# Kernel tuning notes

Hardware: AMD Instinct MI355X
Metric: run time of the kernel (lower is better)

## Reference

```python
import jax, jax.numpy as jnp
import numpy as np

BOS, PAD, EOS, UNK = 0, 1, 2, 3  # fairseq dictionary special-token ids
CHAR_VOCAB = 5000
DIM = 512
LATENT = 10000


def setup_inputs() -> dict:
    key = jax.random.key(0)
    k1, k2, k3 = jax.random.split(key, 3)
    # char-ngram ids per token: [B, T, max_char_len]
    x = jax.random.randint(k1, (8, 1024, 20), 0, CHAR_VOCAB, dtype=jnp.int64 if jax.config.jax_enable_x64 else jnp.int32)
    # char ngram embedding table (also serves as preset_emb for special tokens)
    char_table = jax.random.normal(k2, (CHAR_VOCAB, DIM), dtype=jnp.float32) * 0.05
    # fixed latent codebook, init std = latent**-0.5 as in the module
    latent_mat = jax.random.normal(k3, (LATENT, DIM), dtype=jnp.float32) * (LATENT ** -0.5)
    return {"x": x, "char_table": char_table, "latent_mat": latent_mat}


def reference(x, char_table, latent_mat):
    # --- CharacterNgramEmbedder: gather + sum-pool over char ngrams (pad masked) ---
    emb = char_table[x]                                   # [B, T, C, D]
    valid = (x != PAD)[..., None].astype(emb.dtype)       # pad ngrams contribute 0
    ngram_weight = jnp.sum(emb * valid, axis=2)           # [B, T, D]
    lang_emb = jnp.tanh(ngram_weight)

    # --- latent codebook attention: QK^T -> softmax -> V over fixed codebook ---
    latent_scores = jnp.einsum('btd,ld->btl', lang_emb, latent_mat)   # [B, T, L]
    latent_dist = jax.nn.softmax(latent_scores, axis=-1)
    latent_emb = jnp.einsum('btl,ld->btd', latent_dist, latent_mat)   # [B, T, D]
    sde_emb = lang_emb + latent_emb

    # --- preset_emb overwrite for special tokens (masked scatter) ---
    first = x[:, :, 0]                                    # [B, T]
    for tok in (PAD, BOS, EOS, UNK):
        sde_emb = jnp.where((first == tok)[..., None], char_table[tok], sde_emb)
    return sde_emb
```

## Files before the change

### kernel.cpp

```cpp
#include <hip/hip_runtime.h>

#define BT    8192
#define DIM   512
#define NLAT  10000
#define LPAD2 10240
#define NG    20
#define CV    5000

typedef short bf16x8 __attribute__((ext_vector_type(8)));
typedef float f32x4  __attribute__((ext_vector_type(4)));
typedef unsigned short u16;
typedef u16 u16x8 __attribute__((ext_vector_type(8)));
typedef u16 u16x4 __attribute__((ext_vector_type(4)));

static __device__ __forceinline__ u16 f2bf(float f) {
    union { float f; unsigned u; } v; v.f = f;
    unsigned r = v.u + 0x7FFF + ((v.u >> 16) & 1);
    return (u16)(r >> 16);
}
static __device__ __forceinline__ float bf2f(u16 b) {
    union { unsigned u; float f; } v; v.u = ((unsigned)b) << 16; return v.f;
}

static __device__ __forceinline__ void gload16(const void* g, void* l) {
    __builtin_amdgcn_global_load_lds(
        (const __attribute__((address_space(1))) unsigned int*)g,
        (__attribute__((address_space(3))) unsigned int*)l,
        16, 0, 0);
}

__global__ __launch_bounds__(256) void ct2bf_kernel(
        const float* __restrict__ ct, u16* __restrict__ ctb) {
    const long base = ((long)blockIdx.x * 256 + threadIdx.x) * 8;
    float4 a = *(const float4*)(ct + base);
    float4 b = *(const float4*)(ct + base + 4);
    u16x8 v = { f2bf(a.x), f2bf(a.y), f2bf(a.z), f2bf(a.w),
                f2bf(b.x), f2bf(b.y), f2bf(b.z), f2bf(b.w) };
    *(u16x8*)(ctb + base) = v;
}

__global__ __launch_bounds__(256) void lang_kernel(
        const int* __restrict__ x, const u16* __restrict__ ctb,
        float* __restrict__ lang, u16* __restrict__ qb) {
    const int wv  = threadIdx.x >> 6;
    const int tl  = threadIdx.x & 63;
    const int tok0 = blockIdx.x * 8 + wv * 2;
    const int* xr0 = x + tok0 * NG;
    const int* xr1 = xr0 + NG;
    float s0[8], s1[8];
    #pragma unroll
    for (int i = 0; i < 8; ++i) { s0[i] = 0.f; s1[i] = 0.f; }
    #pragma unroll
    for (int j = 0; j < NG; ++j) {
        int c0 = xr0[j], c1 = xr1[j];
        if (c0 != 1) {
            u16x8 v = *(const u16x8*)(ctb + (long)c0 * DIM + tl * 8);
            #pragma unroll
            for (int i = 0; i < 8; ++i) s0[i] += bf2f(v[i]);
        }
        if (c1 != 1) {
            u16x8 v = *(const u16x8*)(ctb + (long)c1 * DIM + tl * 8);
            #pragma unroll
            for (int i = 0; i < 8; ++i) s1[i] += bf2f(v[i]);
        }
    }
    #pragma unroll
    for (int p = 0; p < 2; ++p) {
        float* s = p ? s1 : s0;
        const long tok = tok0 + p;
        float4 lo, hi;
        lo.x = tanhf(s[0]); lo.y = tanhf(s[1]); lo.z = tanhf(s[2]); lo.w = tanhf(s[3]);
        hi.x = tanhf(s[4]); hi.y = tanhf(s[5]); hi.z = tanhf(s[6]); hi.w = tanhf(s[7]);
        *(float4*)(lang + tok * DIM + tl * 8)     = lo;
        *(float4*)(lang + tok * DIM + tl * 8 + 4) = hi;
        u16x8 o = { f2bf(lo.x), f2bf(lo.y), f2bf(lo.z), f2bf(lo.w),
                    f2bf(hi.x), f2bf(hi.y), f2bf(hi.z), f2bf(hi.w) };
        *(u16x8*)(qb + tok * DIM + tl * 8) = o;
    }
}

__global__ __launch_bounds__(256) void conv_kernel(
        const float* __restrict__ lm, u16* __restrict__ kvg, u16* __restrict__ latT) {
    __shared__ u16 tile[64][514];
    const int lb = blockIdx.x * 64;
    const int t  = threadIdx.x;

    #pragma unroll 4
    for (int i = 0; i < 16; ++i) {
        int ch  = t + i * 256;
        int r   = ch >> 6;
        int c8  = ch & 63;
        int row = lb + r;
        u16x8 v = {0,0,0,0,0,0,0,0};
        if (row < NLAT) {
            const float* src = lm + (long)row * DIM + c8 * 8;
            float4 a = *(const float4*)src;
            float4 b = *(const float4*)(src + 4);
            v[0]=f2bf(a.x); v[1]=f2bf(a.y); v[2]=f2bf(a.z); v[3]=f2bf(a.w);
            v[4]=f2bf(b.x); v[5]=f2bf(b.y); v[6]=f2bf(b.z); v[7]=f2bf(b.w);
        }
        *(u16x8*)(kvg + (long)row * DIM + c8 * 8) = v;
        #pragma unroll
        for (int j = 0; j < 8; ++j) tile[r][c8 * 8 + j] = v[j];
    }
    __syncthreads();
    #pragma unroll 4
    for (int i = 0; i < 16; ++i) {
        int ch = t + i * 256;
        int d  = ch >> 3;
        int c8 = ch & 7;
        u16x8 v;
        #pragma unroll
        for (int j = 0; j < 8; ++j) v[j] = tile[c8 * 8 + j][d];
        *(u16x8*)(latT + (long)d * LPAD2 + lb + c8 * 8) = v;
    }
}

#define G1_COMPUTE(buf) {                                                      \
    bf16x8 af_[4], bf_[4];                                                     \
    _Pragma("unroll")                                                          \
    for (int mf_ = 0; mf_ < 4; ++mf_) {                                        \
        const int rA_ = wm * 64 + mf_ * 16 + lr;                               \
        const int ck_ = g ^ ((rA_ >> 1) & 3);                                  \
        af_[mf_] = *(const bf16x8*)&lds[buf][rA_ * 32 + ck_ * 8];              \
    }                                                                          \
    _Pragma("unroll")                                                          \
    for (int nf_ = 0; nf_ < 4; ++nf_) {                                        \
        const int rB_ = wn * 64 + nf_ * 16 + lr;                               \
        const int ck_ = g ^ ((rB_ >> 1) & 3);                                  \
        bf_[nf_] = *(const bf16x8*)&lds[buf][8192 + rB_ * 32 + ck_ * 8];       \
    }                                                                          \
    __builtin_amdgcn_s_setprio(1);                                             \
    _Pragma("unroll")                                                          \
    for (int mf_ = 0; mf_ < 4; ++mf_)                                          \
        _Pragma("unroll")                                                      \
        for (int nf_ = 0; nf_ < 4; ++nf_)                                      \
            acc[mf_][nf_] = __builtin_amdgcn_mfma_f32_16x16x32_bf16(           \
                af_[mf_], bf_[nf_], acc[mf_][nf_], 0, 0, 0);                   \
    __builtin_amdgcn_s_setprio(0);                                             \
}

#define G1_STAGE(buf, kt) {                                                    \
    const int k0_ = (kt) * 32;                                                 \
    {                                                                          \
        int ch_ = t;                                                           \
        int row_ = ch_ >> 2, c2_ = ch_ & 3;                                    \
        int sc_ = (c2_ ^ ((row_ >> 1) & 3)) * 8;                               \
        gload16(Q + (m0 + row_) * (long)DIM + k0_ + sc_, &lds[buf][ch_ * 8]);  \
        ch_ = t + 512; row_ = ch_ >> 2; c2_ = ch_ & 3;                         \
        sc_ = (c2_ ^ ((row_ >> 1) & 3)) * 8;                                   \
        gload16(Q + (m0 + row_) * (long)DIM + k0_ + sc_, &lds[buf][ch_ * 8]);  \
        row_ = t >> 2; c2_ = t & 3;                                            \
        sc_ = (c2_ ^ ((row_ >> 1) & 3)) * 8;                                   \
        gload16(Bgp + (long)row_ * DIM + k0_ + sc_, &lds[buf][8192 + t * 8]);  \
    }                                                                          \
}

#define G1_STEP(kt, vmn) {                                                     \
    asm volatile("s_waitcnt vmcnt(" #vmn ")" ::: "memory");                    \
    __builtin_amdgcn_s_barrier();                                              \
    G1_COMPUTE((kt) % 3);                                                      \
    __builtin_amdgcn_s_barrier();                                              \
}

__global__ __launch_bounds__(512, 4) void gemm1_kernel(
        const u16* __restrict__ Q, const u16* __restrict__ L,
        u16* __restrict__ P, float* __restrict__ rowsum,
        int n0_global, int npanels, int pstride) {
    __shared__ u16 lds[3][12288];

    const int nwg = 32 * npanels;
    const int cpx = nwg >> 3;
    const int bid = blockIdx.x;
    const int wg  = (bid & 7) * cpx + (bid >> 3);
    int mb, nb;
    if (npanels == 80) {
        const int st = wg / 80, lt = wg % 80;
        const int lmb = lt & 7, lnb = lt >> 3;
        const int smb = st & 3, snb = st >> 2;
        mb = smb * 8 + lmb;
        nb = snb * 10 + lnb;
    } else {
        mb = wg & 31;
        nb = wg >> 5;
    }
    const long m0    = (long)mb * 256;
    const int  ncol0 = n0_global + nb * 128;

    const u16* Bgp = L + (long)ncol0 * DIM;

    const int t = threadIdx.x, lane = t & 63, w = t >> 6;
    const int wm = w >> 1, wn = w & 1;
    const int g = lane >> 4, lr = lane & 15;

    f32x4 acc[4][4];
    #pragma unroll
    for (int m = 0; m < 4; ++m)
        #pragma unroll
        for (int n = 0; n < 4; ++n) acc[m][n] = f32x4{0.f,0.f,0.f,0.f};

    G1_STAGE(0, 0);
    G1_STAGE(1, 1);
    G1_STAGE(2, 2);

    #pragma unroll 1
    for (int kt = 0; kt < 13; ++kt) {
        asm volatile("s_waitcnt vmcnt(6)" ::: "memory");
        __builtin_amdgcn_s_barrier();
        G1_COMPUTE(kt % 3);
        __builtin_amdgcn_s_barrier();
        G1_STAGE(kt % 3, kt + 3);
    }
    G1_STEP(13, 6);
    G1_STEP(14, 3);
    asm volatile("s_waitcnt vmcnt(0)" ::: "memory");
    __builtin_amdgcn_s_barrier();
    G1_COMPUTE(15 % 3);
    __syncthreads();

    u16* lds16 = &lds[0][0];
    #pragma unroll
    for (int mf = 0; mf < 4; ++mf)
        #pragma unroll
        for (int nf = 0; nf < 4; ++nf) {
            const int col = ncol0 + wn * 64 + nf * 16 + lr;
            const bool ok = (col < NLAT);
            const int lcol = wn * 64 + nf * 16 + lr;
            #pragma unroll
            for (int r = 0; r < 4; ++r) {
                float p = ok ? __expf(acc[mf][nf][r]) : 0.f;
                acc[mf][nf][r] = p;
                const int row = wm * 64 + mf * 16 + g * 4 + r;
                lds16[row * 128 + (lcol ^ ((row & 15) << 3))] = f2bf(p);
            }
        }

    #pragma unroll
    for (int mf = 0; mf < 4; ++mf) {
        float sv[4] = {0.f, 0.f, 0.f, 0.f};
        #pragma unroll
        for (int nf = 0; nf < 4; ++nf)
            #pragma unroll
            for (int r = 0; r < 4; ++r) sv[r] += acc[mf][nf][r];
        #pragma unroll
        for (int r = 0; r < 4; ++r) {
            float s = sv[r];
            s += __shfl_xor(s, 1); s += __shfl_xor(s, 2);
            s += __shfl_xor(s, 4); s += __shfl_xor(s, 8);
            if (lr == 0)
                atomicAdd(&rowsum[m0 + wm * 64 + mf * 16 + g * 4 + r], s);
        }
    }

    __syncthreads();
    const int pbase = ncol0 - n0_global;
    #pragma unroll
    for (int it = 0; it < 8; ++it) {
        const int flat = t + it * 512;
        const int row = flat >> 4, ck = flat & 15;
        u16x8 v = *(const u16x8*)&lds16[row * 128 + ((ck ^ (row & 15)) * 8)];
        *(u16x8*)(P + (m0 + row) * (long)pstride + pbase + ck * 8) = v;
    }
}

#define G2_STAGE(buf, kt) {                                                    \
    const int kloc_ = (step_off + (kt)) * 32;                                  \
    {                                                                          \
        int ch_ = t;                                                           \
        int row_ = ch_ >> 2, c2_ = ch_ & 3;                                    \
        int sc_ = (c2_ ^ ((row_ >> 1) & 3)) * 8;                               \
        gload16(P + (m0 + row_) * (long)pstride + kloc_ + sc_, &lds[buf][ch_ * 8]); \
        ch_ = t + 512; row_ = ch_ >> 2; c2_ = ch_ & 3;                         \
        sc_ = (c2_ ^ ((row_ >> 1) & 3)) * 8;                                   \
        gload16(P + (m0 + row_) * (long)pstride + kloc_ + sc_, &lds[buf][ch_ * 8]); \
        row_ = t >> 2; c2_ = t & 3;                                            \
        sc_ = (c2_ ^ ((row_ >> 1) & 3)) * 8;                                   \
        gload16(LT + (long)(nbase + row_) * LPAD2 + n0_global + kloc_ + sc_,   \
                &lds[buf][8192 + t * 8]);                                      \
    }                                                                          \
}

__global__ __launch_bounds__(512, 4) void gemm2_kernel(
        const u16* __restrict__ P, const u16* __restrict__ LT,
        float* __restrict__ out, float* __restrict__ parts,
        int pstride, int kcols, int n0_global, int splitk, int accum) {
    __shared__ u16 lds[3][12288];

    const int per = 4 * splitk;
    const int nwg = 32 * per;
    const int cpx = nwg >> 3;
    const int bid = blockIdx.x;
    const int wg  = (bid & 7) * cpx + (bid >> 3);
    const int mb  = wg / per;
    const int inr = wg % per;
    const int nb  = inr / splitk;
    const int s   = inr % splitk;

    const long m0    = (long)mb * 256;
    const int  nbase = nb * 128;

    const int nsteps = kcols / 32;
    const int q = nsteps / splitk, rr = nsteps % splitk;
    const int NT       = q + (s < rr ? 1 : 0);
    const int step_off = s * q + (s < rr ? s : rr);

    const int t = threadIdx.x, lane = t & 63, w = t >> 6;
    const int wm = w >> 1, wn = w & 1;
    const int g = lane >> 4, lr = lane & 15;

    float* buf = (s == 0) ? out : (parts + (long)(s - 1) * BT * DIM);

    f32x4 acc[4][4];
    #pragma unroll
    for (int m = 0; m < 4; ++m)
        #pragma unroll
        for (int n = 0; n < 4; ++n) acc[m][n] = f32x4{0.f,0.f,0.f,0.f};

    G2_STAGE(0, 0);
    G2_STAGE(1, 1);
    G2_STAGE(2, 2);

    #pragma unroll 1
    for (int kt = 0; kt < NT - 3; ++kt) {
        asm volatile("s_waitcnt vmcnt(6)" ::: "memory");
        __builtin_amdgcn_s_barrier();
        G1_COMPUTE(kt % 3);
        __builtin_amdgcn_s_barrier();
        G2_STAGE(kt % 3, kt + 3);
    }
    {
        asm volatile("s_waitcnt vmcnt(6)" ::: "memory");
        __builtin_amdgcn_s_barrier();
        G1_COMPUTE((NT - 3) % 3);
        __builtin_amdgcn_s_barrier();
    }
    {
        asm volatile("s_waitcnt vmcnt(3)" ::: "memory");
        __builtin_amdgcn_s_barrier();
        G1_COMPUTE((NT - 2) % 3);
        __builtin_amdgcn_s_barrier();
    }
    asm volatile("s_waitcnt vmcnt(0)" ::: "memory");
    __builtin_amdgcn_s_barrier();
    G1_COMPUTE((NT - 1) % 3);

    #pragma unroll
    for (int mf = 0; mf < 4; ++mf)
        #pragma unroll
        for (int nf = 0; nf < 4; ++nf) {
            const int col = nbase + wn * 64 + nf * 16 + lr;
            #pragma unroll
            for (int r = 0; r < 4; ++r) {
                const long row = m0 + wm * 64 + mf * 16 + g * 4 + r;
                float v = acc[mf][nf][r];
                if (accum) v += buf[row * DIM + col];
                buf[row * DIM + col] = v;
            }
        }
}

__global__ __launch_bounds__(256) void final_kernel(
        float* __restrict__ out, const float* __restrict__ parts,
        const float* __restrict__ lang, const float* __restrict__ rowsum,
        const int* __restrict__ x, const float* __restrict__ ct, int nparts) {
    const int tok   = blockIdx.x * 2 + (threadIdx.x >> 7);
    const int c4    = (threadIdx.x & 127) * 4;
    const long idx  = (long)tok * DIM + c4;
    const float inv = 1.f / rowsum[tok];
    const int first = x[tok * NG];

    float4 v = *(const float4*)(out + idx);
    for (int p = 1; p < nparts; ++p) {
        float4 pv = *(const float4*)(parts + (long)(p - 1) * BT * DIM + idx);
        v.x += pv.x; v.y += pv.y; v.z += pv.z; v.w += pv.w;
    }
    float4 lg = *(const float4*)(lang + idx);
    v.x = v.x * inv + lg.x; v.y = v.y * inv + lg.y;
    v.z = v.z * inv + lg.z; v.w = v.w * inv + lg.w;
    if (first < 4) v = *(const float4*)(ct + first * DIM + c4);
    *(float4*)(out + idx) = v;
}

extern "C" void kernel_launch(void* const* d_in, const int* in_sizes, int n_in,
                              void* d_out, int out_size, void* d_ws, size_t ws_size,
                              hipStream_t stream) {
    const int*   x  = (const int*)d_in[0];
    const float* ct = (const float*)d_in[1];
    const float* lm = (const float*)d_in[2];
    float* out = (float*)d_out;

    char* ws = (char*)d_ws;
    size_t off = 0;
    u16*   qb   = (u16*)(ws + off);   off += (size_t)BT * DIM * 2;
    float* lang = (float*)(ws + off); off += (size_t)BT * DIM * 4;
    u16*   kvg  = (u16*)(ws + off);   off += (size_t)LPAD2 * DIM * 2;
    u16*   latT = (u16*)(ws + off);   off += (size_t)DIM * LPAD2 * 2;
    u16*   ctb  = (u16*)(ws + off);   off += (size_t)CV * DIM * 2;
    float* rowsum = (float*)(ws + off); off += (size_t)BT * 4;
    u16*   P    = (u16*)(ws + off);
    const size_t fixed = off;

    const int panels_total = LPAD2 / 128;
    const size_t pfull = (size_t)BT * LPAD2 * 2;
    const size_t partb = (size_t)BT * DIM * 4;

    int splitk = 1, ppc = panels_total;
    float* parts = out;
    if (ws_size >= fixed + pfull + 3 * partb) {
        splitk = 4;
        parts = (float*)(ws + fixed + pfull);
    } else if (ws_size >= fixed + pfull + partb) {
        splitk = 2;
        parts = (float*)(ws + fixed + pfull);
    } else if (ws_size >= fixed + pfull) {
        splitk = 1;
    } else {
        size_t avail = (ws_size > fixed) ? (ws_size - fixed) : 0;
        size_t p = avail / ((size_t)BT * 128 * 2);
        ppc = (int)(p < 1 ? 1 : (p > (size_t)panels_total ? (size_t)panels_total : p));
        if (ppc & 1) ppc = (ppc > 1) ? ppc - 1 : 1;
    }
    const int pstride = ppc * 128;

    hipMemsetAsync(rowsum, 0, (size_t)BT * 4, stream);
    ct2bf_kernel<<<CV * DIM / (256 * 8), 256, 0, stream>>>(ct, ctb);
    lang_kernel<<<BT / 8, 256, 0, stream>>>(x, ctb, lang, qb);
    conv_kernel<<<LPAD2 / 64, 256, 0, stream>>>(lm, kvg, latT);

    int chunk = 0;
    for (int cs = 0; cs < panels_total; cs += ppc, ++chunk) {
        const int np = (panels_total - cs < ppc) ? (panels_total - cs) : ppc;
        gemm1_kernel<<<32 * np, 512, 0, stream>>>(qb, kvg, P, rowsum,
                                                  cs * 128, np, pstride);
        gemm2_kernel<<<32 * 4 * splitk, 512, 0, stream>>>(P, latT, out, parts,
                                                          pstride, np * 128, cs * 128,
                                                          splitk, chunk > 0 ? 1 : 0);
    }
    final_kernel<<<BT / 2, 256, 0, stream>>>(out, parts, lang, rowsum, x, ct, splitk);
}
```

Before: 270.8 us.

## Restructure gemm2 into 256x256 tiles with quarter-phase pipelined loads

The second GEMM (softmax probabilities times latent codebook) now uses 256x256 output tiles with a K-step of 64 instead of 256x128 tiles with a K-step of 32. It double-buffers in a 128KB LDS array split into four half-slots. Each K-step is split into four compute phases, and each phase issues the global-to-LDS load for one upcoming half-slot, interleaving loads with MFMA work. The change also raises the MFMA priority with s_setprio and lowers occupancy to 2 workgroups per CU. The aim is to raise arithmetic intensity per LDS byte and hide load latency, at the cost of more registers, fewer workgroups and more barriers per step.

```diff
diff --git a/kernel.cpp b/kernel.cpp
--- a/kernel.cpp
+++ b/kernel.cpp
@@ -263,30 +263,73 @@
     }
 }
 
-#define G2_STAGE(buf, kt) {                                                    \
-    const int kloc_ = (step_off + (kt)) * 32;                                  \
-    {                                                                          \
-        int ch_ = t;                                                           \
-        int row_ = ch_ >> 2, c2_ = ch_ & 3;                                    \
-        int sc_ = (c2_ ^ ((row_ >> 1) & 3)) * 8;                               \
-        gload16(P + (m0 + row_) * (long)pstride + kloc_ + sc_, &lds[buf][ch_ * 8]); \
-        ch_ = t + 512; row_ = ch_ >> 2; c2_ = ch_ & 3;                         \
-        sc_ = (c2_ ^ ((row_ >> 1) & 3)) * 8;                                   \
-        gload16(P + (m0 + row_) * (long)pstride + kloc_ + sc_, &lds[buf][ch_ * 8]); \
-        row_ = t >> 2; c2_ = t & 3;                                            \
-        sc_ = (c2_ ^ ((row_ >> 1) & 3)) * 8;                                   \
-        gload16(LT + (long)(nbase + row_) * LPAD2 + n0_global + kloc_ + sc_,   \
-                &lds[buf][8192 + t * 8]);                                      \
-    }                                                                          \
-}
-
-__global__ __launch_bounds__(512, 4) void gemm2_kernel(
+#define SLOT(d, h) ((d) * 32768 + (h) * 8192)
+
+#define G2_STAGE_H(kt2, h) {                                                   \
+    const int d2_ = (kt2) & 1;                                                 \
+    const int kc_ = (step_off + (kt2)) * 64;                                   \
+    _Pragma("unroll")                                                          \
+    for (int i_ = 0; i_ < 2; ++i_) {                                           \
+        int ch_ = t + i_ * 512;                                                \
+        int row_ = ch_ >> 3;                                                   \
+        int sc_ = ((ch_ & 7) ^ (row_ & 7)) * 8;                                \
+        if ((h) < 2) {                                                         \
+            gload16(P + (m0 + (h) * 128 + row_) * (long)pstride + kc_ + sc_,   \
+                    &lds[SLOT(d2_, (h)) + ch_ * 8]);                           \
+        } else {                                                               \
+            gload16(LT + (long)(nbase + ((h) - 2) * 128 + row_) * LPAD2        \
+                        + n0_global + kc_ + sc_,                               \
+                    &lds[SLOT(d2_, (h)) + ch_ * 8]);                           \
+        }                                                                      \
+    }                                                                          \
+}
+
+#define G2_PHASE(kt_, mh_, nh_, skt_, sh_) {                                   \
+    const int d_ = (kt_) & 1;                                                  \
+    bf16x8 af_[4][2], bf_[2][2];                                               \
+    _Pragma("unroll")                                                          \
+    for (int mf_ = 0; mf_ < 4; ++mf_) {                                        \
+        const int ra_ = qr * 64 + mf_ * 16 + lr;                               \
+        _Pragma("unroll")                                                      \
+        for (int kk_ = 0; kk_ < 2; ++kk_)                                      \
+            af_[mf_][kk_] = *(const bf16x8*)&lds[SLOT(d_, (mh_)) + ra_ * 64    \
+                + (((kk_ * 4 + g) ^ (lr & 7)) * 8)];                           \
+    }                                                                          \
+    _Pragma("unroll")                                                          \
+    for (int nf_ = 0; nf_ < 2; ++nf_) {                                        \
+        const int rb_ = qc * 32 + nf_ * 16 + lr;                               \
+        _Pragma("unroll")                                                      \
+        for (int kk_ = 0; kk_ < 2; ++kk_)                                      \
+            bf_[nf_][kk_] = *(const bf16x8*)&lds[SLOT(d_, 2 + (nh_)) + rb_ * 64 \
+                + (((kk_ * 4 + g) ^ (lr & 7)) * 8)];                           \
+    }                                                                          \
+    if ((skt_) >= 2 && (skt_) < NT) G2_STAGE_H((skt_), (sh_));                 \
+    if ((kt_) >= 2 && (kt_) < NT - 2) {                                        \
+        asm volatile("s_waitcnt vmcnt(6)" ::: "memory");                       \
+    } else {                                                                   \
+        asm volatile("s_waitcnt vmcnt(0)" ::: "memory");                       \
+    }                                                                          \
+    __builtin_amdgcn_s_barrier();                                              \
+    __builtin_amdgcn_s_setprio(1);                                             \
+    _Pragma("unroll")                                                          \
+    for (int mf_ = 0; mf_ < 4; ++mf_)                                          \
+        _Pragma("unroll")                                                      \
+        for (int nf_ = 0; nf_ < 2; ++nf_)                                      \
+            _Pragma("unroll")                                                  \
+            for (int kk_ = 0; kk_ < 2; ++kk_)                                  \
+                acc[mh_][nh_][mf_][nf_] = __builtin_amdgcn_mfma_f32_16x16x32_bf16( \
+                    af_[mf_][kk_], bf_[nf_][kk_], acc[mh_][nh_][mf_][nf_], 0, 0, 0); \
+    __builtin_amdgcn_s_setprio(0);                                             \
+    __builtin_amdgcn_s_barrier();                                              \
+}
+
+__global__ __launch_bounds__(512, 2) void gemm2_kernel(
         const u16* __restrict__ P, const u16* __restrict__ LT,
         float* __restrict__ out, float* __restrict__ parts,
         int pstride, int kcols, int n0_global, int splitk, int accum) {
-    __shared__ u16 lds[3][12288];
-
-    const int per = 4 * splitk;
+    __shared__ u16 lds[65536];
+
+    const int per = 2 * splitk;
     const int nwg = 32 * per;
     const int cpx = nwg >> 3;
     const int bid = blockIdx.x;
@@ -297,66 +340,60 @@
     const int s   = inr % splitk;
 
     const long m0    = (long)mb * 256;
-    const int  nbase = nb * 128;
-
-    const int nsteps = kcols / 32;
+    const int  nbase = nb * 256;
+
+    const int nsteps = kcols / 64;
     const int q = nsteps / splitk, rr = nsteps % splitk;
     const int NT       = q + (s < rr ? 1 : 0);
     const int step_off = s * q + (s < rr ? s : rr);
 
     const int t = threadIdx.x, lane = t & 63, w = t >> 6;
-    const int wm = w >> 1, wn = w & 1;
+    const int qr = w >> 2, qc = w & 3;
     const int g = lane >> 4, lr = lane & 15;
 
     float* buf = (s == 0) ? out : (parts + (long)(s - 1) * BT * DIM);
 
-    f32x4 acc[4][4];
-    #pragma unroll
-    for (int m = 0; m < 4; ++m)
-        #pragma unroll
-        for (int n = 0; n < 4; ++n) acc[m][n] = f32x4{0.f,0.f,0.f,0.f};
-
-    G2_STAGE(0, 0);
-    G2_STAGE(1, 1);
-    G2_STAGE(2, 2);
-
-    #pragma unroll 1
-    for (int kt = 0; kt < NT - 3; ++kt) {
-        asm volatile("s_waitcnt vmcnt(6)" ::: "memory");
-        __builtin_amdgcn_s_barrier();
-        G1_COMPUTE(kt % 3);
-        __builtin_amdgcn_s_barrier();
-        G2_STAGE(kt % 3, kt + 3);
-    }
-    {
-        asm volatile("s_waitcnt vmcnt(6)" ::: "memory");
-        __builtin_amdgcn_s_barrier();
-        G1_COMPUTE((NT - 3) % 3);
-        __builtin_amdgcn_s_barrier();
-    }
-    {
-        asm volatile("s_waitcnt vmcnt(3)" ::: "memory");
-        __builtin_amdgcn_s_barrier();
-        G1_COMPUTE((NT - 2) % 3);
-        __builtin_amdgcn_s_barrier();
-    }
+    f32x4 acc[2][2][4][2];
+    #pragma unroll
+    for (int a = 0; a < 2; ++a)
+        #pragma unroll
+        for (int b = 0; b < 2; ++b)
+            #pragma unroll
+            for (int m = 0; m < 4; ++m)
+                #pragma unroll
+                for (int n = 0; n < 2; ++n)
+                    acc[a][b][m][n] = f32x4{0.f,0.f,0.f,0.f};
+
+    G2_STAGE_H(0, 0); G2_STAGE_H(0, 1); G2_STAGE_H(0, 2); G2_STAGE_H(0, 3);
+    if (NT > 1) { G2_STAGE_H(1, 0); G2_STAGE_H(1, 1); G2_STAGE_H(1, 2); G2_STAGE_H(1, 3); }
     asm volatile("s_waitcnt vmcnt(0)" ::: "memory");
     __builtin_amdgcn_s_barrier();
-    G1_COMPUTE((NT - 1) % 3);
-
-    #pragma unroll
-    for (int mf = 0; mf < 4; ++mf)
-        #pragma unroll
-        for (int nf = 0; nf < 4; ++nf) {
-            const int col = nbase + wn * 64 + nf * 16 + lr;
-            #pragma unroll
-            for (int r = 0; r < 4; ++r) {
-                const long row = m0 + wm * 64 + mf * 16 + g * 4 + r;
-                float v = acc[mf][nf][r];
-                if (accum) v += buf[row * DIM + col];
-                buf[row * DIM + col] = v;
-            }
-        }
+
+    #pragma unroll 1
+    for (int kt = 0; kt < NT; ++kt) {
+        G2_PHASE(kt, 0, 0, kt + 1, 1);
+        G2_PHASE(kt, 1, 0, kt + 1, 3);
+        G2_PHASE(kt, 0, 1, kt + 2, 2);
+        G2_PHASE(kt, 1, 1, kt + 2, 0);
+    }
+
+    #pragma unroll
+    for (int mh = 0; mh < 2; ++mh)
+        #pragma unroll
+        for (int nh = 0; nh < 2; ++nh)
+            #pragma unroll
+            for (int mf = 0; mf < 4; ++mf)
+                #pragma unroll
+                for (int nf = 0; nf < 2; ++nf) {
+                    const int col = nbase + nh * 128 + qc * 32 + nf * 16 + lr;
+                    #pragma unroll
+                    for (int r = 0; r < 4; ++r) {
+                        const long row = m0 + mh * 128 + qr * 64 + mf * 16 + g * 4 + r;
+                        float v = acc[mh][nh][mf][nf][r];
+                        if (accum) v += buf[row * DIM + col];
+                        buf[row * DIM + col] = v;
+                    }
+                }
 }
 
 __global__ __launch_bounds__(256) void final_kernel(
@@ -432,7 +469,7 @@
         const int np = (panels_total - cs < ppc) ? (panels_total - cs) : ppc;
         gemm1_kernel<<<32 * np, 512, 0, stream>>>(qb, kvg, P, rowsum,
                                                   cs * 128, np, pstride);
-        gemm2_kernel<<<32 * 4 * splitk, 512, 0, stream>>>(P, latT, out, parts,
+        gemm2_kernel<<<32 * 2 * splitk, 512, 0, stream>>>(P, latT, out, parts,
                                                           pstride, np * 128, cs * 128,
                                                           splitk, chunk > 0 ? 1 : 0);
     }
```

Measured after the change: 355.6 us. 31.3% more time.
